# Optimization experiments

Hardware: AMD Instinct MI355X
Metric: run time of the kernel (lower is better)

The kernel has to match this reference:

```python
import jax, jax.numpy as jnp
import numpy as np

ACT_BITS = 8
W_BITS = 8
BN_EPS = 1e-5


def _round_ste(x):
    # straight-through round (HAWQ-style ste_round)
    return x + jax.lax.stop_gradient(jnp.round(x) - x)


def _quant_sym(x, bits):
    # symmetric per-tensor fake quantization; scale treated as constant (EMA min/max in original)
    n = float(2 ** (bits - 1) - 1)
    s = jax.lax.stop_gradient(jnp.maximum(jnp.max(jnp.abs(x)) / n, 1e-8))
    xq = jnp.clip(_round_ste(x / s), -n - 1.0, n) * s
    return xq, s


def _conv(x, w, stride, pad):
    return jax.lax.conv_general_dilated(
        x, w, (stride, stride), [(pad, pad), (pad, pad)],
        dimension_numbers=("NCHW", "OIHW", "NCHW"))


def _quant_bn(x, gamma, beta, mean, var):
    # fold BN into a per-channel scale+bias; quantize the folded scale like a weight
    ws = gamma * jax.lax.rsqrt(var + BN_EPS)          # [C]
    wq, ws_scale = _quant_sym(ws, W_BITS)
    b = beta - mean * wq                               # [C]
    return x * wq[None, :, None, None] + b[None, :, None, None], ws_scale


def setup_inputs() -> dict:
    key = jax.random.key(0)
    ks = jax.random.split(key, 16)
    d = {}
    d["x"] = jax.random.normal(ks[0], (32, 128, 56, 56), jnp.float32)
    d["w1"] = jax.random.normal(ks[1], (256, 128, 3, 3), jnp.float32) * 0.05
    d["w2"] = jax.random.normal(ks[2], (256, 256, 3, 3), jnp.float32) * 0.05
    d["w_id"] = jax.random.normal(ks[3], (256, 128, 1, 1), jnp.float32) * 0.05
    for i, pfx in enumerate(["bn1", "bn2", "id"]):
        k4 = jax.random.split(ks[4 + i], 4)
        d[pfx + "_gamma"] = jax.random.uniform(k4[0], (256,), jnp.float32) + 0.5
        d[pfx + "_beta"] = jax.random.normal(k4[1], (256,), jnp.float32) * 0.1
        d[pfx + "_mean"] = jax.random.normal(k4[2], (256,), jnp.float32) * 0.1
        d[pfx + "_var"] = jax.random.uniform(k4[3], (256,), jnp.float32) + 0.5
    return d


def reference(x, w1, w2, w_id,
              bn1_gamma, bn1_beta, bn1_mean, bn1_var,
              bn2_gamma, bn2_beta, bn2_mean, bn2_var,
              id_gamma, id_beta, id_mean, id_var):
    # quant_act on block input
    xq, act_s = _quant_sym(x, ACT_BITS)

    # identity branch: 1x1 stride-2 quantized conv -> quant_act -> folded quant bn
    w_id_q, _ = _quant_sym(w_id, W_BITS)
    identity = _conv(xq, w_id_q, 2, 0)
    identity, _ = _quant_sym(identity, ACT_BITS)
    identity, _ = _quant_bn(identity, id_gamma, id_beta, id_mean, id_var)

    # main branch conv1 (3x3 stride 2) -> act quant -> bn -> relu -> act quant
    w1_q, _ = _quant_sym(w1, W_BITS)
    h = _conv(xq, w1_q, 2, 1)
    h, _ = _quant_sym(h, ACT_BITS)
    h, _ = _quant_bn(h, bn1_gamma, bn1_beta, bn1_mean, bn1_var)
    h = jax.nn.relu(h)
    h, _ = _quant_sym(h, ACT_BITS)

    # conv2 (3x3 stride 1) -> act quant -> bn
    w2_q, _ = _quant_sym(w2, W_BITS)
    h = _conv(h, w2_q, 1, 1)
    h, _ = _quant_sym(h, ACT_BITS)
    h, _ = _quant_bn(h, bn2_gamma, bn2_beta, bn2_mean, bn2_var)

    # residual add -> int32 requant -> relu
    h = h + identity
    h, out_s = _quant_sym(h, ACT_BITS)
    h = jax.nn.relu(h)
    return h, out_s
```

## Files before the change

kernel.cpp:

```cpp
#include <hip/hip_runtime.h>
#include <limits.h>

#define THREADS 256
#define TAIL_BLOCKS 896

typedef int vi4 __attribute__((ext_vector_type(4)));

__device__ __forceinline__ float clamp8f(float q) { return fminf(fmaxf(q, -128.0f), 127.0f); }
__device__ __forceinline__ float sc_from_bits(unsigned b) {
  return fmaxf(__uint_as_float(b) / 127.0f, 1e-8f);
}
__device__ __forceinline__ signed char q8(float v, float s) {
  return (signed char)(int)clamp8f(rintf(v / s));
}


__device__ __forceinline__ void amax_body(const float4* __restrict__ p, int n4, int bid,
                                          int nblocks, int* __restrict__ slot) {
  const int tid = threadIdx.x;
  const int stride = nblocks * THREADS;
  float m = 0.0f;
  int i = bid * THREADS + tid;
  for (; i + 3 * stride < n4; i += 4 * stride) {
    float4 v0 = p[i];
    float4 v1 = p[i + stride];
    float4 v2 = p[i + 2 * stride];
    float4 v3 = p[i + 3 * stride];
    float m0 = fmaxf(fmaxf(fabsf(v0.x), fabsf(v0.y)), fmaxf(fabsf(v0.z), fabsf(v0.w)));
    float m1 = fmaxf(fmaxf(fabsf(v1.x), fabsf(v1.y)), fmaxf(fabsf(v1.z), fabsf(v1.w)));
    float m2 = fmaxf(fmaxf(fabsf(v2.x), fabsf(v2.y)), fmaxf(fabsf(v2.z), fabsf(v2.w)));
    float m3 = fmaxf(fmaxf(fabsf(v3.x), fabsf(v3.y)), fmaxf(fabsf(v3.z), fabsf(v3.w)));
    m = fmaxf(m, fmaxf(fmaxf(m0, m1), fmaxf(m2, m3)));
  }
  for (; i < n4; i += stride) {
    float4 v = p[i];
    m = fmaxf(m, fmaxf(fmaxf(fabsf(v.x), fabsf(v.y)), fmaxf(fabsf(v.z), fabsf(v.w))));
  }
#pragma unroll
  for (int k = 32; k >= 1; k >>= 1) m = fmaxf(m, __shfl_xor(m, k));
  __shared__ float wred[4];
  if ((tid & 63) == 0) wred[tid >> 6] = m;
  __syncthreads();
  if (tid == 0) {
    m = fmaxf(fmaxf(wred[0], wred[1]), fmaxf(wred[2], wred[3]));
    atomicMax(slot, __float_as_int(m));
  }
}

__global__ __launch_bounds__(THREADS) void k_pre(
    int* IS, const float* g1, const float* be1, const float* m1, const float* v1, float* wq1,
    float* b1, const float* g2, const float* be2, const float* m2, const float* v2, float* wq2,
    float* b2, const float* gi, const float* bei, const float* mi, const float* vvi, float* wqi,
    float* bi, const float4* w1, const float4* w2, const float4* wid, const float4* x) {
  int b = blockIdx.x;
  int c = threadIdx.x;
  if (b < 3) {
    const float *gamma, *beta, *mean, *var;
    float *wq, *bb;
    if (b == 0) { gamma = g1; beta = be1; mean = m1; var = v1; wq = wq1; bb = b1; }
    else if (b == 1) { gamma = g2; beta = be2; mean = m2; var = v2; wq = wq2; bb = b2; }
    else { gamma = gi; beta = bei; mean = mi; var = vvi; wq = wqi; bb = bi; }
    __shared__ float red[THREADS];
    float ws = gamma[c] * (1.0f / sqrtf(var[c] + 1e-5f));
    red[c] = fabsf(ws);
    __syncthreads();
    for (int s = THREADS / 2; s > 0; s >>= 1) {
      if (c < s) red[c] = fmaxf(red[c], red[c + s]);
      __syncthreads();
    }
    float sws = fmaxf(red[0] / 127.0f, 1e-8f);
    float q = clamp8f(rintf(ws / sws)) * sws;
    wq[c] = q;
    bb[c] = beta[c] - mean[c] * q;
    return;
  }
  b -= 3;
  if (b < 64) { amax_body(w1, 73728, b, 64, IS + 1); return; }
  b -= 64;
  if (b < 128) { amax_body(w2, 147456, b, 128, IS + 2); return; }
  b -= 128;
  if (b < 16) { amax_body(wid, 8192, b, 16, IS + 3); return; }
  b -= 16;
  amax_body(x, 3211264, b, 512, IS + 0);
}

__global__ __launch_bounds__(THREADS) void k_quant(const float* __restrict__ x,
                                                   int* __restrict__ X8,
                                                   const float* __restrict__ w1f,
                                                   vi4* __restrict__ W1m,
                                                   const float* __restrict__ w2f,
                                                   vi4* __restrict__ W2m,
                                                   const float* __restrict__ widf,
                                                   vi4* __restrict__ Widm,
                                                   const unsigned* __restrict__ ISu) {
  __shared__ signed char tile[56 * 132];
  int b = blockIdx.x;
  int t = threadIdx.x;
  if (b < 1792) {
    float s = sc_from_bits(ISu[0]);
    int h = b % 56, n = b / 56;
    const float* xp = x + ((n * 128) * 56 + h) * 56;
#pragma unroll
    for (int k = 0; k < 28; ++k) {
      int i = t + k * 256;
      int w = i % 56, c = i / 56;
      tile[w * 132 + c] = q8(xp[c * 3136 + w], s);
    }
    __syncthreads();
    int* op = X8 + (n * 56 + h) * 56 * 32;
#pragma unroll
    for (int k = 0; k < 7; ++k) {
      int i = t + k * 256;
      int w = i >> 5, c4 = (i & 31) * 4;
      const signed char* tp = tile + w * 132 + c4;
      op[i] = (int)(unsigned char)tp[0] | ((int)(unsigned char)tp[1] << 8) |
              ((int)(unsigned char)tp[2] << 16) | ((int)(unsigned char)tp[3] << 24);
    }
    return;
  }
  if (b < 1864) {
    int tt = (b - 1792) * THREADS + t;
    float s = sc_from_bits(ISu[1]);
    int lane = tt & 63;
    int cotile = (tt >> 6) & 15;
    int ks = tt >> 10;
    int tap = ks >> 1, kc = ks & 1;
    int kh = tap / 3, kw = tap % 3;
    int co = cotile * 16 + (lane & 15);
    int ci0 = kc * 64 + (lane >> 4) * 16;
    const float* src = w1f + (co * 128 + ci0) * 9 + kh * 3 + kw;
    int r[4];
#pragma unroll
    for (int q = 0; q < 4; ++q) {
      unsigned b0 = (unsigned char)q8(src[(q * 4 + 0) * 9], s);
      unsigned b1 = (unsigned char)q8(src[(q * 4 + 1) * 9], s);
      unsigned b2 = (unsigned char)q8(src[(q * 4 + 2) * 9], s);
      unsigned b3 = (unsigned char)q8(src[(q * 4 + 3) * 9], s);
      r[q] = (int)(b0 | (b1 << 8) | (b2 << 16) | (b3 << 24));
    }
    vi4 v = {r[0], r[1], r[2], r[3]};
    W1m[tt] = v;
    return;
  }
  if (b < 2008) {
    int tt = (b - 1864) * THREADS + t;
    float s = sc_from_bits(ISu[2]);
    int lane = tt & 63;
    int cotile = (tt >> 6) & 15;
    int ks = tt >> 10;
    int tap = ks >> 2, kc = ks & 3;
    int kh = tap / 3, kw = tap % 3;
    int co = cotile * 16 + (lane & 15);
    int ci0 = kc * 64 + (lane >> 4) * 16;
    const float* src = w2f + (co * 256 + ci0) * 9 + kh * 3 + kw;
    int r[4];
#pragma unroll
    for (int q = 0; q < 4; ++q) {
      unsigned b0 = (unsigned char)q8(src[(q * 4 + 0) * 9], s);
      unsigned b1 = (unsigned char)q8(src[(q * 4 + 1) * 9], s);
      unsigned b2 = (unsigned char)q8(src[(q * 4 + 2) * 9], s);
      unsigned b3 = (unsigned char)q8(src[(q * 4 + 3) * 9], s);
      r[q] = (int)(b0 | (b1 << 8) | (b2 << 16) | (b3 << 24));
    }
    vi4 v = {r[0], r[1], r[2], r[3]};
    W2m[tt] = v;
    return;
  }
  {
    int tt = (b - 2008) * THREADS + t;
    float s = sc_from_bits(ISu[3]);
    int lane = tt & 63;
    int cotile = (tt >> 6) & 15;
    int ks = tt >> 10;
    int co = cotile * 16 + (lane & 15);
    int ci0 = ks * 64 + (lane >> 4) * 16;
    const float* src = widf + co * 128 + ci0;
    int r[4];
#pragma unroll
    for (int q = 0; q < 4; ++q) {
      unsigned b0 = (unsigned char)q8(src[q * 4 + 0], s);
      unsigned b1 = (unsigned char)q8(src[q * 4 + 1], s);
      unsigned b2 = (unsigned char)q8(src[q * 4 + 2], s);
      unsigned b3 = (unsigned char)q8(src[q * 4 + 3], s);
      r[q] = (int)(b0 | (b1 << 8) | (b2 << 16) | (b3 << 24));
    }
    vi4 v = {r[0], r[1], r[2], r[3]};
    Widm[tt] = v;
  }
}

#define MFMA_I8(a, b, c) __builtin_amdgcn_mfma_i32_16x16x64_i8(a, b, c, 0, 0, 0)

__global__ __launch_bounds__(THREADS, 3) void k_conv1(const int* __restrict__ X8,
                                                      const vi4* __restrict__ W1m,
                                                      const vi4* __restrict__ Widm,
                                                      int* __restrict__ H1, int* __restrict__ IDI,
                                                      int* __restrict__ maxS,
                                                      int* __restrict__ minS,
                                                      int* __restrict__ maxabs_id) {
  __shared__ __align__(16) int lds[5 * 58 * 36];
  __shared__ int sMax[2][128], sMin[2][128], redA[4];
  const int tid = threadIdx.x;
  const int bx = blockIdx.x;
  const int n = bx / 28, rr = bx % 28;
  const int hp = rr >> 1, nh = rr & 1;
  const int ho0 = hp * 2;
  vi4 zero = {0, 0, 0, 0};

  for (int r = 0; r < 5; ++r) {
    int h = 2 * ho0 - 1 + r;
    int* dst = lds + r * 58 * 36;
    if (h >= 0 && h < 56) {
      const vi4* src = (const vi4*)(X8 + (n * 56 + h) * 56 * 32);
      for (int i4 = tid; i4 < 448; i4 += THREADS) {
        int col = i4 >> 3, c = (i4 & 7) * 4;
        *(vi4*)(dst + (col + 1) * 36 + c) = src[i4];
      }
      if (tid < 32) dst[tid] = 0;
      else if (tid >= 128 && tid < 160) dst[57 * 36 + (tid - 128)] = 0;
    } else {
      for (int i4 = tid; i4 < 522; i4 += THREADS) ((vi4*)dst)[i4] = zero;
    }
  }
  __syncthreads();

  const int lane = tid & 63, wv = tid >> 6;
  const int mw = wv & 1, nw = wv >> 1;
  const int lm = lane & 15, quad = lane >> 4;
  const int woc0 = lm, woc1 = (16 + lm) > 27 ? 27 : (16 + lm);
  const int choff = quad * 4;
  const int ho = ho0 + mw;
  const int obase = ((n * 28 + ho) * 28) * 256;
  const int ctbase = nh * 8 + nw * 4;

  vi4 acc[2][4];
  vi4 bA[4], bB[4];
  vi4 a0A, a1A, a0B, a1B;

#pragma unroll
  for (int mt = 0; mt < 2; ++mt)
#pragma unroll
    for (int ct = 0; ct < 4; ++ct) acc[mt][ct] = zero;
  const vi4* wibase = Widm + ctbase * 64 + lane;
  {
    const int ro = (2 * mw + 1) * 58;
#pragma unroll
    for (int kc = 0; kc < 2; ++kc) {
      vi4 a0 = *(const vi4*)(lds + (ro + 2 * woc0 + 1) * 36 + kc * 16 + choff);
      vi4 a1 = *(const vi4*)(lds + (ro + 2 * woc1 + 1) * 36 + kc * 16 + choff);
#pragma unroll
      for (int ct = 0; ct < 4; ++ct) {
        vi4 b = wibase[kc * 1024 + ct * 64];
        acc[0][ct] = MFMA_I8(a0, b, acc[0][ct]);
        acc[1][ct] = MFMA_I8(a1, b, acc[1][ct]);
      }
    }
  }
  int am = 0;
#pragma unroll
  for (int ct = 0; ct < 4; ++ct) {
    const int co = (ctbase + ct) * 16 + lm;
#pragma unroll
    for (int mt = 0; mt < 2; ++mt)
#pragma unroll
      for (int r = 0; r < 4; ++r) {
        int wo = mt * 16 + quad * 4 + r;
        if (wo < 28) {
          int v = acc[mt][ct][r];
          IDI[obase + wo * 256 + co] = v;
          am = max(am, v < 0 ? -v : v);
        }
      }
  }
#pragma unroll
  for (int k = 32; k >= 1; k >>= 1) am = max(am, __shfl_xor(am, k));
  if (lane == 0) redA[wv] = am;

#pragma unroll
  for (int mt = 0; mt < 2; ++mt)
#pragma unroll
    for (int ct = 0; ct < 4; ++ct) acc[mt][ct] = zero;
  const vi4* wbase = W1m + ctbase * 64 + lane;
#pragma unroll
  for (int ct = 0; ct < 4; ++ct) bA[ct] = wbase[ct * 64];
  {
    const int ro = (2 * mw) * 58;
    a0A = *(const vi4*)(lds + (ro + 2 * woc0) * 36 + choff);
    a1A = *(const vi4*)(lds + (ro + 2 * woc1) * 36 + choff);
  }
#pragma unroll 1
  for (int ks = 0; ks < 18; ks += 2) {
    {
      const int ksn = ks + 1;
      const int khn = (ksn >= 6) + (ksn >= 12);
      const int t2 = ksn - khn * 6;
      const int kwn = t2 >> 1, kcn = t2 & 1;
#pragma unroll
      for (int ct = 0; ct < 4; ++ct) bB[ct] = wbase[ksn * 1024 + ct * 64];
      const int ro = (2 * mw + khn) * 58;
      a0B = *(const vi4*)(lds + (ro + 2 * woc0 + kwn) * 36 + kcn * 16 + choff);
      a1B = *(const vi4*)(lds + (ro + 2 * woc1 + kwn) * 36 + kcn * 16 + choff);
    }
#pragma unroll
    for (int ct = 0; ct < 4; ++ct) {
      acc[0][ct] = MFMA_I8(a0A, bA[ct], acc[0][ct]);
      acc[1][ct] = MFMA_I8(a1A, bA[ct], acc[1][ct]);
    }
    if (ks + 2 < 18) {
      const int ksn = ks + 2;
      const int khn = (ksn >= 6) + (ksn >= 12);
      const int t2 = ksn - khn * 6;
      const int kwn = t2 >> 1, kcn = t2 & 1;
#pragma unroll
      for (int ct = 0; ct < 4; ++ct) bA[ct] = wbase[ksn * 1024 + ct * 64];
      const int ro = (2 * mw + khn) * 58;
      a0A = *(const vi4*)(lds + (ro + 2 * woc0 + kwn) * 36 + kcn * 16 + choff);
      a1A = *(const vi4*)(lds + (ro + 2 * woc1 + kwn) * 36 + kcn * 16 + choff);
    }
#pragma unroll
    for (int ct = 0; ct < 4; ++ct) {
      acc[0][ct] = MFMA_I8(a0B, bB[ct], acc[0][ct]);
      acc[1][ct] = MFMA_I8(a1B, bB[ct], acc[1][ct]);
    }
  }

#pragma unroll
  for (int ct = 0; ct < 4; ++ct) {
    const int co = (ctbase + ct) * 16 + lm;
    int vmax = INT_MIN, vmin = INT_MAX;
#pragma unroll
    for (int mt = 0; mt < 2; ++mt)
#pragma unroll
      for (int r = 0; r < 4; ++r) {
        int wo = mt * 16 + quad * 4 + r;
        if (wo < 28) {
          int v = acc[mt][ct][r];
          H1[obase + wo * 256 + co] = v;
          vmax = max(vmax, v);
          vmin = min(vmin, v);
        }
      }
    vmax = max(vmax, __shfl_xor(vmax, 16));
    vmax = max(vmax, __shfl_xor(vmax, 32));
    vmin = min(vmin, __shfl_xor(vmin, 16));
    vmin = min(vmin, __shfl_xor(vmin, 32));
    if (lane < 16) {
      sMax[mw][nw * 64 + ct * 16 + lane] = vmax;
      sMin[mw][nw * 64 + ct * 16 + lane] = vmin;
    }
  }
  __syncthreads();
  if (tid < 128) {
    int row = n * 14 + hp;
    maxS[row * 256 + nh * 128 + tid] = max(sMax[0][tid], sMax[1][tid]);
    minS[row * 256 + nh * 128 + tid] = min(sMin[0][tid], sMin[1][tid]);
  }
  if (tid == 0) {
    int a = max(max(redA[0], redA[1]), max(redA[2], redA[3]));
    atomicMax(maxabs_id, a);
  }
}

__global__ __launch_bounds__(1024) void k_rs1(int* __restrict__ IS, float* __restrict__ SC,
                                              const int* __restrict__ maxS,
                                              const int* __restrict__ minS,
                                              const float* __restrict__ wq1,
                                              const float* __restrict__ b1) {
  __shared__ int pMax[4][256], pMin[4][256];
  __shared__ int ri[256];
  __shared__ float rf[256];
  int t = threadIdx.x;
  if (t < 320) IS[128 + t] = 0;
  int c = t & 255, part = t >> 8;
  int vmax = INT_MIN, vmin = INT_MAX;
#pragma unroll 4
  for (int r = part; r < 448; r += 4) {
    vmax = max(vmax, maxS[r * 256 + c]);
    vmin = min(vmin, minS[r * 256 + c]);
  }
  pMax[part][c] = vmax;
  pMin[part][c] = vmin;
  __syncthreads();
  if (t < 256) {
    vmax = max(max(pMax[0][c], pMax[1][c]), max(pMax[2][c], pMax[3][c]));
    vmin = min(min(pMin[0][c], pMin[1][c]), min(pMin[2][c], pMin[3][c]));
    int a1 = vmax < 0 ? -vmax : vmax;
    int a0 = vmin < 0 ? -vmin : vmin;
    ri[c] = max(a1, a0);
  }
  __syncthreads();
  for (int s = 128; s > 0; s >>= 1) {
    if (t < s) ri[t] = max(ri[t], ri[t + s]);
    __syncthreads();
  }
  int mh1 = ri[0];
  const unsigned* ISu = (const unsigned*)IS;
  float sx = sc_from_bits(ISu[0]);
  float sw1 = sc_from_bits(ISu[1]);
  float sxw = sx * sw1;
  float s_h1 = fmaxf(sxw * (float)mh1 / 127.0f, 1e-8f);
  if (t < 256) {
    float wq = wq1[c], bbc = b1[c];
    float q1 = clamp8f(rintf((float)vmax * sxw / s_h1));
    float q0 = clamp8f(rintf((float)vmin * sxw / s_h1));
    float hv1 = q1 * s_h1, hv0 = q0 * s_h1;
    float y1 = fmaxf(hv1 * wq + bbc, 0.0f);
    float y0 = fmaxf(hv0 * wq + bbc, 0.0f);
    rf[c] = fmaxf(y1, y0);
  }
  __syncthreads();
  for (int s = 128; s > 0; s >>= 1) {
    if (t < s) rf[t] = fmaxf(rf[t], rf[t + s]);
    __syncthreads();
  }
  if (t == 0) {
    IS[4] = mh1;
    SC[7] = rf[0];
    SC[8] = s_h1;
    SC[9] = fmaxf(rf[0] / 127.0f, 1e-8f);
    float swid = sc_from_bits(ISu[3]);
    SC[10] = fmaxf(sx * swid * (float)IS[5] / 127.0f, 1e-8f);
  }
}

__device__ __forceinline__ signed char qact(int v, float sxw, float s_h1, float s_y2, float wq,
                                            float bb) {
  float hf = (float)v * sxw;
  float q = clamp8f(rintf(hf / s_h1));
  float hv = q * s_h1;
  float y = fmaxf(hv * wq + bb, 0.0f);
  float a = fminf(fmaxf(rintf(y / s_y2), -128.0f), 127.0f);
  return (signed char)(int)a;
}

__global__ __launch_bounds__(THREADS) void k_qh1(const int4* __restrict__ H1,
                                                 char4* __restrict__ A2,
                                                 const float* __restrict__ SC,
                                                 const float* __restrict__ wq1,
                                                 const float* __restrict__ b1) {
  int t = blockIdx.x * THREADS + threadIdx.x;
  const unsigned* ISu = (const unsigned*)SC;
  float sx = sc_from_bits(ISu[0]);
  float sw1 = sc_from_bits(ISu[1]);
  float sxw = sx * sw1;
  float s_h1 = SC[8];
  float s_y2 = SC[9];
  int4 v = H1[t];
  int c0 = (t * 4) & 255;
  char4 r;
  r.x = qact(v.x, sxw, s_h1, s_y2, wq1[c0], b1[c0]);
  r.y = qact(v.y, sxw, s_h1, s_y2, wq1[c0 + 1], b1[c0 + 1]);
  r.z = qact(v.z, sxw, s_h1, s_y2, wq1[c0 + 2], b1[c0 + 2]);
  r.w = qact(v.w, sxw, s_h1, s_y2, wq1[c0 + 3], b1[c0 + 3]);
  A2[t] = r;
}

struct SumParams {
  float sxw2, s_h2, sxwid, s_idq;
};
__device__ __forceinline__ float sum_val(int v2, int vi, const SumParams& P, float wq2c, float b2c,
                                         float wqidc, float bidc) {
  float q2 = clamp8f(rintf((float)v2 * P.sxw2 / P.s_h2));
  float z = (q2 * P.s_h2) * wq2c + b2c;
  float qi = clamp8f(rintf((float)vi * P.sxwid / P.s_idq));
  float zi = (qi * P.s_idq) * wqidc + bidc;
  return z + zi;
}
__device__ __forceinline__ SumParams make_params2(const float* SC, const unsigned* ISu, int mh2) {
  SumParams P;
  float sx = sc_from_bits(ISu[0]);
  float sw2 = sc_from_bits(ISu[2]);
  float swid = sc_from_bits(ISu[3]);
  float s_y2 = SC[9];
  P.s_idq = SC[10];
  P.sxw2 = s_y2 * sw2;
  P.s_h2 = fmaxf(P.sxw2 * (float)mh2 / 127.0f, 1e-8f);
  P.sxwid = sx * swid;
  return P;
}

__global__ __launch_bounds__(THREADS, 4) void k_tail(const int* __restrict__ A2,
                                                     const vi4* __restrict__ W2m,
                                                     const int* __restrict__ IDI,
                                                     const float* SC, int* IS,
                                                     const float* __restrict__ wq2,
                                                     const float* __restrict__ b2,
                                                     const float* __restrict__ wqid,
                                                     const float* __restrict__ bidp,
                                                     float* __restrict__ out) {
  __shared__ __align__(16) int lds[4 * 30 * 68];
  __shared__ int redA[4];
  __shared__ float redF[4];
  __shared__ int sMh2;
  __shared__ float sOutS;
  const int tid = threadIdx.x;
  const int bx = blockIdx.x;
  const int n = bx / 28, rr = bx % 28;
  const int hp = rr >> 1, nh = rr & 1;
  const int ho0 = hp * 2;
  vi4 zero = {0, 0, 0, 0};

  for (int r = 0; r < 4; ++r) {
    int h = ho0 - 1 + r;
    int* dst = lds + r * 30 * 68;
    if (h >= 0 && h < 28) {
      const vi4* src = (const vi4*)(A2 + (n * 28 + h) * 28 * 64);
      for (int i4 = tid; i4 < 448; i4 += THREADS) {
        int col = i4 >> 4, c = (i4 & 15) * 4;
        *(vi4*)(dst + (col + 1) * 68 + c) = src[i4];
      }
      if (tid < 64) dst[tid] = 0;
      else if (tid >= 128 && tid < 192) dst[29 * 68 + (tid - 128)] = 0;
    } else {
      for (int i4 = tid; i4 < 510; i4 += THREADS) ((vi4*)dst)[i4] = zero;
    }
  }
  __syncthreads();

  const int lane = tid & 63, wv = tid >> 6;
  const int mw = wv & 1, nw = wv >> 1;
  const int lm = lane & 15, quad = lane >> 4;
  const int woc0 = lm, woc1 = (16 + lm) > 27 ? 27 : (16 + lm);
  const int choff = quad * 4;
  const int ctbase = nh * 8 + nw * 4;

  vi4 acc[2][4];
  vi4 bA[4], bB[4];
  vi4 a0A, a1A, a0B, a1B;
#pragma unroll
  for (int mt = 0; mt < 2; ++mt)
#pragma unroll
    for (int ct = 0; ct < 4; ++ct) acc[mt][ct] = zero;

  const vi4* wbase = W2m + ctbase * 64 + lane;
#pragma unroll
  for (int ct = 0; ct < 4; ++ct) bA[ct] = wbase[ct * 64];
  {
    const int ro = mw * 30;
    a0A = *(const vi4*)(lds + (ro + woc0) * 68 + choff);
    a1A = *(const vi4*)(lds + (ro + woc1) * 68 + choff);
  }
#pragma unroll 1
  for (int ks = 0; ks < 36; ks += 2) {
    {
      const int ksn = ks + 1;
      const int khn = (ksn >= 12) + (ksn >= 24);
      const int t2 = ksn - khn * 12;
      const int kwn = t2 >> 2, kcn = t2 & 3;
#pragma unroll
      for (int ct = 0; ct < 4; ++ct) bB[ct] = wbase[ksn * 1024 + ct * 64];
      const int ro = (mw + khn) * 30;
      a0B = *(const vi4*)(lds + (ro + woc0 + kwn) * 68 + kcn * 16 + choff);
      a1B = *(const vi4*)(lds + (ro + woc1 + kwn) * 68 + kcn * 16 + choff);
    }
#pragma unroll
    for (int ct = 0; ct < 4; ++ct) {
      acc[0][ct] = MFMA_I8(a0A, bA[ct], acc[0][ct]);
      acc[1][ct] = MFMA_I8(a1A, bA[ct], acc[1][ct]);
    }
    if (ks + 2 < 36) {
      const int ksn = ks + 2;
      const int khn = (ksn >= 12) + (ksn >= 24);
      const int t2 = ksn - khn * 12;
      const int kwn = t2 >> 2, kcn = t2 & 3;
#pragma unroll
      for (int ct = 0; ct < 4; ++ct) bA[ct] = wbase[ksn * 1024 + ct * 64];
      const int ro = (mw + khn) * 30;
      a0A = *(const vi4*)(lds + (ro + woc0 + kwn) * 68 + kcn * 16 + choff);
      a1A = *(const vi4*)(lds + (ro + woc1 + kwn) * 68 + kcn * 16 + choff);
    }
#pragma unroll
    for (int ct = 0; ct < 4; ++ct) {
      acc[0][ct] = MFMA_I8(a0B, bB[ct], acc[0][ct]);
      acc[1][ct] = MFMA_I8(a1B, bB[ct], acc[1][ct]);
    }
  }

  int am = 0;
#pragma unroll
  for (int ct = 0; ct < 4; ++ct)
#pragma unroll
    for (int mt = 0; mt < 2; ++mt)
#pragma unroll
      for (int r = 0; r < 4; ++r) {
        int wo = mt * 16 + quad * 4 + r;
        if (wo < 28) {
          int v = acc[mt][ct][r];
          am = max(am, v < 0 ? -v : v);
        }
      }
#pragma unroll
  for (int k = 32; k >= 1; k >>= 1) am = max(am, __shfl_xor(am, k));
  if (lane == 0) redA[wv] = am;
  __syncthreads();
  if (tid == 0) {
    int a = max(max(redA[0], redA[1]), max(redA[2], redA[3]));
    atomicMax(IS + 6, a);
  }

  int* sumsi = lds;
  float* sums = (float*)lds;
  const int ib = ((n * 28 + ho0) * 28) * 256 + nh * 128;
#pragma unroll
  for (int k = 0; k < 28; ++k) {
    int idx = tid + k * 256;
    int cl = idx & 127, sp = idx >> 7;
    sumsi[cl * 57 + sp] = IDI[ib + sp * 256 + cl];
  }
  __syncthreads();

  if (tid == 0) {
    asm volatile("s_waitcnt vmcnt(0)" ::: "memory");
    int old = __hip_atomic_fetch_add(IS + 128 + (bx & 7) * 16, 1, __ATOMIC_RELAXED,
                                     __HIP_MEMORY_SCOPE_AGENT);
    if (old == 111) {
      int r = __hip_atomic_fetch_add(IS + 256, 1, __ATOMIC_RELAXED, __HIP_MEMORY_SCOPE_AGENT);
      if (r == 7)
        __hip_atomic_fetch_add(IS + 272, 1, __ATOMIC_RELAXED, __HIP_MEMORY_SCOPE_AGENT);
    }
    while (__hip_atomic_load(IS + 272, __ATOMIC_RELAXED, __HIP_MEMORY_SCOPE_SYSTEM) == 0)
      __builtin_amdgcn_s_sleep(2);
    sMh2 = __hip_atomic_load(IS + 6, __ATOMIC_RELAXED, __HIP_MEMORY_SCOPE_SYSTEM);
  }
  __syncthreads();
  const SumParams P = make_params2(SC, (const unsigned*)IS, sMh2);

  float fm = 0.0f;
#pragma unroll
  for (int ct = 0; ct < 4; ++ct) {
    const int co = (ctbase + ct) * 16 + lm;
    const int cl = co - nh * 128;
    float w2c = wq2[co], b2c = b2[co], wic = wqid[co], bic = bidp[co];
#pragma unroll
    for (int mt = 0; mt < 2; ++mt)
#pragma unroll
      for (int r = 0; r < 4; ++r) {
        int wo = mt * 16 + quad * 4 + r;
        if (wo < 28) {
          int slot = cl * 57 + mw * 28 + wo;
          float sv = sum_val(acc[mt][ct][r], sumsi[slot], P, w2c, b2c, wic, bic);
          sums[slot] = sv;
          fm = fmaxf(fm, fabsf(sv));
        }
      }
  }
#pragma unroll
  for (int k = 32; k >= 1; k >>= 1) fm = fmaxf(fm, __shfl_xor(fm, k));
  if (lane == 0) redF[wv] = fm;
  __syncthreads();

  if (tid == 0) {
    float a = fmaxf(fmaxf(redF[0], redF[1]), fmaxf(redF[2], redF[3]));
    atomicMax(IS + 11, __float_as_int(a));
    asm volatile("s_waitcnt vmcnt(0)" ::: "memory");
    int old = __hip_atomic_fetch_add(IS + 288 + (bx & 7) * 16, 1, __ATOMIC_RELAXED,
                                     __HIP_MEMORY_SCOPE_AGENT);
    if (old == 111) {
      int r = __hip_atomic_fetch_add(IS + 416, 1, __ATOMIC_RELAXED, __HIP_MEMORY_SCOPE_AGENT);
      if (r == 7)
        __hip_atomic_fetch_add(IS + 432, 1, __ATOMIC_RELAXED, __HIP_MEMORY_SCOPE_AGENT);
    }
    while (__hip_atomic_load(IS + 432, __ATOMIC_RELAXED, __HIP_MEMORY_SCOPE_SYSTEM) == 0)
      __builtin_amdgcn_s_sleep(2);
    int mb = __hip_atomic_load(IS + 11, __ATOMIC_RELAXED, __HIP_MEMORY_SCOPE_SYSTEM);
    sOutS = fmaxf(__int_as_float(mb) / 127.0f, 1e-8f);
  }
  __syncthreads();
  const float out_s = sOutS;

  float* ob = out + n * 200704 + (nh * 128) * 784 + ho0 * 28;
#pragma unroll
  for (int k = 0; k < 28; ++k) {
    int idx = tid + k * 256;
    int cl = idx / 56, rem = idx % 56;
    float sv = sums[cl * 57 + rem];
    float q = clamp8f(rintf(sv / out_s));
    ob[cl * 784 + rem] = q > 0.0f ? q * out_s : 0.0f;
  }
  if (bx == 0 && tid == 0) out[6422528] = out_s;
}

extern "C" void kernel_launch(void* const* d_in, const int* in_sizes, int n_in, void* d_out,
                              int out_size, void* d_ws, size_t ws_size, hipStream_t stream) {
  (void)in_sizes; (void)n_in; (void)out_size; (void)ws_size;
  const float* x = (const float*)d_in[0];
  const float* w1 = (const float*)d_in[1];
  const float* w2 = (const float*)d_in[2];
  const float* wid = (const float*)d_in[3];
  const float* bn1g = (const float*)d_in[4];
  const float* bn1b = (const float*)d_in[5];
  const float* bn1m = (const float*)d_in[6];
  const float* bn1v = (const float*)d_in[7];
  const float* bn2g = (const float*)d_in[8];
  const float* bn2b = (const float*)d_in[9];
  const float* bn2m = (const float*)d_in[10];
  const float* bn2v = (const float*)d_in[11];
  const float* idg = (const float*)d_in[12];
  const float* idb = (const float*)d_in[13];
  const float* idm = (const float*)d_in[14];
  const float* idv = (const float*)d_in[15];

  char* ws = (char*)d_ws;
  float* SC = (float*)ws;
  int* IS = (int*)ws;
  unsigned* ISu = (unsigned*)ws;
  float* wq1 = (float*)(ws + 3072);
  float* b1 = (float*)(ws + 4096);
  float* wq2 = (float*)(ws + 5120);
  float* b2 = (float*)(ws + 6144);
  float* wqid = (float*)(ws + 7168);
  float* bid = (float*)(ws + 8192);
  char* X8 = ws + 16384;
  char* A2 = X8;
  char* W1m = X8 + 12845056;
  char* W2m = W1m + 294912;
  char* Widm = W2m + 589824;
  int* H1 = (int*)(Widm + 32768);
  int* IDI = (int*)((char*)H1 + 25690112);
  float* out = (float*)d_out;
  int* maxS = (int*)d_out;
  int* minS = maxS + 448 * 256;

  k_pre<<<723, THREADS, 0, stream>>>(IS, bn1g, bn1b, bn1m, bn1v, wq1, b1, bn2g, bn2b, bn2m, bn2v,
                                     wq2, b2, idg, idb, idm, idv, wqid, bid, (const float4*)w1,
                                     (const float4*)w2, (const float4*)wid, (const float4*)x);
  k_quant<<<2016, THREADS, 0, stream>>>(x, (int*)X8, w1, (vi4*)W1m, w2, (vi4*)W2m, wid,
                                        (vi4*)Widm, ISu);
  k_conv1<<<896, THREADS, 0, stream>>>((const int*)X8, (const vi4*)W1m, (const vi4*)Widm, H1, IDI,
                                       maxS, minS, IS + 5);
  k_rs1<<<1, 1024, 0, stream>>>(IS, SC, maxS, minS, wq1, b1);
  k_qh1<<<6272, THREADS, 0, stream>>>((const int4*)H1, (char4*)A2, SC, wq1, b1);
  k_tail<<<TAIL_BLOCKS, THREADS, 0, stream>>>((const int*)A2, (const vi4*)W2m, (const int*)IDI, SC,
                                              IS, wq2, b2, wqid, bid, out);
}
```

Measured before the change: 249.5 us.

## Fuse conv1, scale reduction and activation requant into one persistent kernel

Merges k_conv1, k_rs1 and k_qh1 into a single 896-block kernel that keeps the int32 conv1 outputs in LDS, uses software grid barriers to compute the per-channel min/max and the activation scales, then writes the int8 A2 tensor directly. This removes the 25 MB H1 int32 round-trip through global memory and two kernel launches, including a single-block reduction kernel. The LDS input tile also switches from padded rows to an XOR-swizzled layout, and occupancy is raised to 4 blocks per SM. The cost is three grid-wide spin barriers, which depend on all 896 blocks being co-resident and can deadlock if they are not.

Measured after the change: 246.9 us. No clear change (-1.0%).

```diff
diff --git a/kernel.cpp b/kernel.cpp
--- a/kernel.cpp
+++ b/kernel.cpp
@@ -2,7 +2,7 @@
 #include <limits.h>
 
 #define THREADS 256
-#define TAIL_BLOCKS 896
+#define GRID_BLOCKS 896
 
 typedef int vi4 __attribute__((ext_vector_type(4)));
 
@@ -14,6 +14,19 @@
   return (signed char)(int)clamp8f(rintf(v / s));
 }
 
+
+__device__ __forceinline__ void gbar(int* IS, int base, int bx) {
+  asm volatile("s_waitcnt vmcnt(0)" ::: "memory");
+  int old = __hip_atomic_fetch_add(IS + base + (bx & 7) * 16, 1, __ATOMIC_RELAXED,
+                                   __HIP_MEMORY_SCOPE_AGENT);
+  if (old == 111) {
+    int r = __hip_atomic_fetch_add(IS + base + 128, 1, __ATOMIC_RELAXED, __HIP_MEMORY_SCOPE_AGENT);
+    if (r == 7)
+      __hip_atomic_fetch_add(IS + base + 144, 1, __ATOMIC_RELAXED, __HIP_MEMORY_SCOPE_AGENT);
+  }
+  while (__hip_atomic_load(IS + base + 144, __ATOMIC_RELAXED, __HIP_MEMORY_SCOPE_SYSTEM) == 0)
+    __builtin_amdgcn_s_sleep(2);
+}
 
 __device__ __forceinline__ void amax_body(const float4* __restrict__ p, int n4, int bid,
                                           int nblocks, int* __restrict__ slot) {
@@ -55,6 +68,12 @@
   int b = blockIdx.x;
   int c = threadIdx.x;
   if (b < 3) {
+    if (b == 0) {
+      IS[128 + c] = 0;
+      IS[384 + c] = 0;
+      IS[640 + c] = 0;
+      if (c < 32) IS[896 + c] = 0;
+    }
     const float *gamma, *beta, *mean, *var;
     float *wq, *bb;
     if (b == 0) { gamma = g1; beta = be1; mean = m1; var = v1; wq = wq1; bb = b1; }
@@ -191,15 +210,26 @@
 
 #define MFMA_I8(a, b, c) __builtin_amdgcn_mfma_i32_16x16x64_i8(a, b, c, 0, 0, 0)
 
-__global__ __launch_bounds__(THREADS, 3) void k_conv1(const int* __restrict__ X8,
-                                                      const vi4* __restrict__ W1m,
-                                                      const vi4* __restrict__ Widm,
-                                                      int* __restrict__ H1, int* __restrict__ IDI,
-                                                      int* __restrict__ maxS,
-                                                      int* __restrict__ minS,
-                                                      int* __restrict__ maxabs_id) {
-  __shared__ __align__(16) int lds[5 * 58 * 36];
-  __shared__ int sMax[2][128], sMin[2][128], redA[4];
+__device__ __forceinline__ signed char qact(int v, float sxw, float s_h1, float s_y2, float wq,
+                                            float bb) {
+  float hf = (float)v * sxw;
+  float q = clamp8f(rintf(hf / s_h1));
+  float hv = q * s_h1;
+  float y = fmaxf(hv * wq + bb, 0.0f);
+  float a = fminf(fmaxf(rintf(y / s_y2), -128.0f), 127.0f);
+  return (signed char)(int)a;
+}
+
+__global__ __launch_bounds__(THREADS, 4) void k_cv1(const int* X8, const vi4* __restrict__ W1m,
+                                                    const vi4* __restrict__ Widm,
+                                                    int* __restrict__ IDI, int* A2i, int* IS,
+                                                    const float* __restrict__ wq1,
+                                                    const float* __restrict__ b1, float* SC,
+                                                    int* maxS2, int* minS2) {
+  __shared__ __align__(16) int lds[9280];
+  __shared__ int redA[4];
+  __shared__ int sVmax, sVmin;
+  __shared__ float sSxw, sSh1, sSy2;
   const int tid = threadIdx.x;
   const int bx = blockIdx.x;
   const int n = bx / 28, rr = bx % 28;
@@ -209,17 +239,18 @@
 
   for (int r = 0; r < 5; ++r) {
     int h = 2 * ho0 - 1 + r;
-    int* dst = lds + r * 58 * 36;
+    int* dst = lds + r * 58 * 32;
     if (h >= 0 && h < 56) {
       const vi4* src = (const vi4*)(X8 + (n * 56 + h) * 56 * 32);
       for (int i4 = tid; i4 < 448; i4 += THREADS) {
-        int col = i4 >> 3, c = (i4 & 7) * 4;
-        *(vi4*)(dst + (col + 1) * 36 + c) = src[i4];
+        int col = i4 >> 3, e0 = (i4 & 7) * 4;
+        int cell = r * 58 + col + 1;
+        *(vi4*)(lds + cell * 32 + (e0 ^ ((cell & 7) << 2))) = src[i4];
       }
       if (tid < 32) dst[tid] = 0;
-      else if (tid >= 128 && tid < 160) dst[57 * 36 + (tid - 128)] = 0;
+      else if (tid >= 128 && tid < 160) dst[57 * 32 + (tid - 128)] = 0;
     } else {
-      for (int i4 = tid; i4 < 522; i4 += THREADS) ((vi4*)dst)[i4] = zero;
+      for (int i4 = tid; i4 < 464; i4 += THREADS) ((vi4*)dst)[i4] = zero;
     }
   }
   __syncthreads();
@@ -233,6 +264,10 @@
   const int obase = ((n * 28 + ho) * 28) * 256;
   const int ctbase = nh * 8 + nw * 4;
 
+#define LDA(row, colp, sub)                                                              \
+  (*(const vi4*)(lds + ((row) * 58 + (colp)) * 32 +                                      \
+                 ((sub) ^ ((((row) * 58 + (colp)) & 7) << 2))))
+
   vi4 acc[2][4];
   vi4 bA[4], bB[4];
   vi4 a0A, a1A, a0B, a1B;
@@ -243,11 +278,11 @@
     for (int ct = 0; ct < 4; ++ct) acc[mt][ct] = zero;
   const vi4* wibase = Widm + ctbase * 64 + lane;
   {
-    const int ro = (2 * mw + 1) * 58;
+    const int row = 2 * mw + 1;
 #pragma unroll
     for (int kc = 0; kc < 2; ++kc) {
-      vi4 a0 = *(const vi4*)(lds + (ro + 2 * woc0 + 1) * 36 + kc * 16 + choff);
-      vi4 a1 = *(const vi4*)(lds + (ro + 2 * woc1 + 1) * 36 + kc * 16 + choff);
+      vi4 a0 = LDA(row, 2 * woc0 + 1, kc * 16 + choff);
+      vi4 a1 = LDA(row, 2 * woc1 + 1, kc * 16 + choff);
 #pragma unroll
       for (int ct = 0; ct < 4; ++ct) {
         vi4 b = wibase[kc * 1024 + ct * 64];
@@ -284,9 +319,8 @@
 #pragma unroll
   for (int ct = 0; ct < 4; ++ct) bA[ct] = wbase[ct * 64];
   {
-    const int ro = (2 * mw) * 58;
-    a0A = *(const vi4*)(lds + (ro + 2 * woc0) * 36 + choff);
-    a1A = *(const vi4*)(lds + (ro + 2 * woc1) * 36 + choff);
+    a0A = LDA(2 * mw, 2 * woc0, choff);
+    a1A = LDA(2 * mw, 2 * woc1, choff);
   }
 #pragma unroll 1
   for (int ks = 0; ks < 18; ks += 2) {
@@ -297,9 +331,9 @@
       const int kwn = t2 >> 1, kcn = t2 & 1;
 #pragma unroll
       for (int ct = 0; ct < 4; ++ct) bB[ct] = wbase[ksn * 1024 + ct * 64];
-      const int ro = (2 * mw + khn) * 58;
-      a0B = *(const vi4*)(lds + (ro + 2 * woc0 + kwn) * 36 + kcn * 16 + choff);
-      a1B = *(const vi4*)(lds + (ro + 2 * woc1 + kwn) * 36 + kcn * 16 + choff);
+      const int row = 2 * mw + khn;
+      a0B = LDA(row, 2 * woc0 + kwn, kcn * 16 + choff);
+      a1B = LDA(row, 2 * woc1 + kwn, kcn * 16 + choff);
     }
 #pragma unroll
     for (int ct = 0; ct < 4; ++ct) {
@@ -313,9 +347,9 @@
       const int kwn = t2 >> 1, kcn = t2 & 1;
 #pragma unroll
       for (int ct = 0; ct < 4; ++ct) bA[ct] = wbase[ksn * 1024 + ct * 64];
-      const int ro = (2 * mw + khn) * 58;
-      a0A = *(const vi4*)(lds + (ro + 2 * woc0 + kwn) * 36 + kcn * 16 + choff);
-      a1A = *(const vi4*)(lds + (ro + 2 * woc1 + kwn) * 36 + kcn * 16 + choff);
+      const int row = 2 * mw + khn;
+      a0A = LDA(row, 2 * woc0 + kwn, kcn * 16 + choff);
+      a1A = LDA(row, 2 * woc1 + kwn, kcn * 16 + choff);
     }
 #pragma unroll
     for (int ct = 0; ct < 4; ++ct) {
@@ -326,7 +360,6 @@
 
 #pragma unroll
   for (int ct = 0; ct < 4; ++ct) {
-    const int co = (ctbase + ct) * 16 + lm;
     int vmax = INT_MIN, vmin = INT_MAX;
 #pragma unroll
     for (int mt = 0; mt < 2; ++mt)
@@ -335,7 +368,6 @@
         int wo = mt * 16 + quad * 4 + r;
         if (wo < 28) {
           int v = acc[mt][ct][r];
-          H1[obase + wo * 256 + co] = v;
           vmax = max(vmax, v);
           vmin = min(vmin, v);
         }
@@ -345,114 +377,132 @@
     vmin = min(vmin, __shfl_xor(vmin, 16));
     vmin = min(vmin, __shfl_xor(vmin, 32));
     if (lane < 16) {
-      sMax[mw][nw * 64 + ct * 16 + lane] = vmax;
-      sMin[mw][nw * 64 + ct * 16 + lane] = vmin;
-    }
-  }
-  __syncthreads();
-  if (tid < 128) {
-    int row = n * 14 + hp;
-    maxS[row * 256 + nh * 128 + tid] = max(sMax[0][tid], sMax[1][tid]);
-    minS[row * 256 + nh * 128 + tid] = min(sMin[0][tid], sMin[1][tid]);
-  }
+      int cl = (nw * 4 + ct) * 16 + lane;
+      __hip_atomic_store(maxS2 + bx * 256 + mw * 128 + cl, vmax, __ATOMIC_RELAXED,
+                         __HIP_MEMORY_SCOPE_AGENT);
+      __hip_atomic_store(minS2 + bx * 256 + mw * 128 + cl, vmin, __ATOMIC_RELAXED,
+                         __HIP_MEMORY_SCOPE_AGENT);
+    }
+  }
+
+  __syncthreads();
   if (tid == 0) {
     int a = max(max(redA[0], redA[1]), max(redA[2], redA[3]));
-    atomicMax(maxabs_id, a);
-  }
-}
-
-__global__ __launch_bounds__(1024) void k_rs1(int* __restrict__ IS, float* __restrict__ SC,
-                                              const int* __restrict__ maxS,
-                                              const int* __restrict__ minS,
-                                              const float* __restrict__ wq1,
-                                              const float* __restrict__ b1) {
-  __shared__ int pMax[4][256], pMin[4][256];
-  __shared__ int ri[256];
-  __shared__ float rf[256];
-  int t = threadIdx.x;
-  if (t < 320) IS[128 + t] = 0;
-  int c = t & 255, part = t >> 8;
-  int vmax = INT_MIN, vmin = INT_MAX;
-#pragma unroll 4
-  for (int r = part; r < 448; r += 4) {
-    vmax = max(vmax, maxS[r * 256 + c]);
-    vmin = min(vmin, minS[r * 256 + c]);
-  }
-  pMax[part][c] = vmax;
-  pMin[part][c] = vmin;
-  __syncthreads();
-  if (t < 256) {
-    vmax = max(max(pMax[0][c], pMax[1][c]), max(pMax[2][c], pMax[3][c]));
-    vmin = min(min(pMin[0][c], pMin[1][c]), min(pMin[2][c], pMin[3][c]));
-    int a1 = vmax < 0 ? -vmax : vmax;
-    int a0 = vmin < 0 ? -vmin : vmin;
-    ri[c] = max(a1, a0);
-  }
-  __syncthreads();
-  for (int s = 128; s > 0; s >>= 1) {
-    if (t < s) ri[t] = max(ri[t], ri[t + s]);
+    atomicMax(IS + 5, a);
+  }
+#pragma unroll
+  for (int ct = 0; ct < 4; ++ct) {
+    const int cl = (nw * 4 + ct) * 16 + lm;
+#pragma unroll
+    for (int mt = 0; mt < 2; ++mt)
+#pragma unroll
+      for (int r = 0; r < 4; ++r) {
+        int wo = mt * 16 + quad * 4 + r;
+        if (wo < 28) lds[(mw * 28 + wo) * 130 + cl] = acc[mt][ct][r];
+      }
+  }
+  __syncthreads();
+  if (tid == 0) gbar(IS, 128, bx);
+  __syncthreads();
+
+  if (bx < 256) {
+    const int c = bx, nhc = c >> 7, cl = c & 127;
+    int vmax = INT_MIN, vmin = INT_MAX;
+    for (int j = tid; j < 896; j += THREADS) {
+      int bxx = nhc + ((j >> 1) << 1);
+      int mwj = j & 1;
+      int a = __hip_atomic_load(maxS2 + bxx * 256 + mwj * 128 + cl, __ATOMIC_RELAXED,
+                                __HIP_MEMORY_SCOPE_AGENT);
+      int i_ = __hip_atomic_load(minS2 + bxx * 256 + mwj * 128 + cl, __ATOMIC_RELAXED,
+                                 __HIP_MEMORY_SCOPE_AGENT);
+      vmax = max(vmax, a);
+      vmin = min(vmin, i_);
+    }
+    int* rMax = lds + 7280;
+    int* rMin = lds + 7536;
+    rMax[tid] = vmax;
+    rMin[tid] = vmin;
     __syncthreads();
-  }
-  int mh1 = ri[0];
-  const unsigned* ISu = (const unsigned*)IS;
-  float sx = sc_from_bits(ISu[0]);
-  float sw1 = sc_from_bits(ISu[1]);
-  float sxw = sx * sw1;
-  float s_h1 = fmaxf(sxw * (float)mh1 / 127.0f, 1e-8f);
-  if (t < 256) {
-    float wq = wq1[c], bbc = b1[c];
-    float q1 = clamp8f(rintf((float)vmax * sxw / s_h1));
-    float q0 = clamp8f(rintf((float)vmin * sxw / s_h1));
-    float hv1 = q1 * s_h1, hv0 = q0 * s_h1;
-    float y1 = fmaxf(hv1 * wq + bbc, 0.0f);
-    float y0 = fmaxf(hv0 * wq + bbc, 0.0f);
-    rf[c] = fmaxf(y1, y0);
-  }
-  __syncthreads();
-  for (int s = 128; s > 0; s >>= 1) {
-    if (t < s) rf[t] = fmaxf(rf[t], rf[t + s]);
-    __syncthreads();
-  }
-  if (t == 0) {
-    IS[4] = mh1;
-    SC[7] = rf[0];
-    SC[8] = s_h1;
-    SC[9] = fmaxf(rf[0] / 127.0f, 1e-8f);
-    float swid = sc_from_bits(ISu[3]);
-    SC[10] = fmaxf(sx * swid * (float)IS[5] / 127.0f, 1e-8f);
-  }
-}
-
-__device__ __forceinline__ signed char qact(int v, float sxw, float s_h1, float s_y2, float wq,
-                                            float bb) {
-  float hf = (float)v * sxw;
-  float q = clamp8f(rintf(hf / s_h1));
-  float hv = q * s_h1;
-  float y = fmaxf(hv * wq + bb, 0.0f);
-  float a = fminf(fmaxf(rintf(y / s_y2), -128.0f), 127.0f);
-  return (signed char)(int)a;
-}
-
-__global__ __launch_bounds__(THREADS) void k_qh1(const int4* __restrict__ H1,
-                                                 char4* __restrict__ A2,
-                                                 const float* __restrict__ SC,
-                                                 const float* __restrict__ wq1,
-                                                 const float* __restrict__ b1) {
-  int t = blockIdx.x * THREADS + threadIdx.x;
-  const unsigned* ISu = (const unsigned*)SC;
-  float sx = sc_from_bits(ISu[0]);
-  float sw1 = sc_from_bits(ISu[1]);
-  float sxw = sx * sw1;
-  float s_h1 = SC[8];
-  float s_y2 = SC[9];
-  int4 v = H1[t];
-  int c0 = (t * 4) & 255;
-  char4 r;
-  r.x = qact(v.x, sxw, s_h1, s_y2, wq1[c0], b1[c0]);
-  r.y = qact(v.y, sxw, s_h1, s_y2, wq1[c0 + 1], b1[c0 + 1]);
-  r.z = qact(v.z, sxw, s_h1, s_y2, wq1[c0 + 2], b1[c0 + 2]);
-  r.w = qact(v.w, sxw, s_h1, s_y2, wq1[c0 + 3], b1[c0 + 3]);
-  A2[t] = r;
+    for (int s = 128; s > 0; s >>= 1) {
+      if (tid < s) {
+        rMax[tid] = max(rMax[tid], rMax[tid + s]);
+        rMin[tid] = min(rMin[tid], rMin[tid + s]);
+      }
+      __syncthreads();
+    }
+    if (tid == 0) {
+      sVmax = rMax[0];
+      sVmin = rMin[0];
+      int a1 = sVmax < 0 ? -sVmax : sVmax;
+      int a0 = sVmin < 0 ? -sVmin : sVmin;
+      atomicMax(IS + 4, max(a1, a0));
+    }
+  }
+  __syncthreads();
+  if (tid == 0) gbar(IS, 288, bx);
+  __syncthreads();
+
+  if (bx < 256 && tid == 0) {
+    float sx = sc_from_bits((unsigned)__hip_atomic_load(IS + 0, __ATOMIC_RELAXED,
+                                                        __HIP_MEMORY_SCOPE_AGENT));
+    float sw1 = sc_from_bits((unsigned)__hip_atomic_load(IS + 1, __ATOMIC_RELAXED,
+                                                         __HIP_MEMORY_SCOPE_AGENT));
+    int mh1 = __hip_atomic_load(IS + 4, __ATOMIC_RELAXED, __HIP_MEMORY_SCOPE_AGENT);
+    float sxw = sx * sw1;
+    float s_h1 = fmaxf(sxw * (float)mh1 / 127.0f, 1e-8f);
+    float wq = wq1[bx], bbc = b1[bx];
+    float q1 = clamp8f(rintf((float)sVmax * sxw / s_h1));
+    float q0 = clamp8f(rintf((float)sVmin * sxw / s_h1));
+    float y1 = fmaxf(q1 * s_h1 * wq + bbc, 0.0f);
+    float y0 = fmaxf(q0 * s_h1 * wq + bbc, 0.0f);
+    atomicMax(IS + 7, __float_as_int(fmaxf(y1, y0)));
+  }
+  __syncthreads();
+  if (tid == 0) gbar(IS, 448, bx);
+  __syncthreads();
+
+  if (tid == 0) {
+    float sx = sc_from_bits((unsigned)__hip_atomic_load(IS + 0, __ATOMIC_RELAXED,
+                                                        __HIP_MEMORY_SCOPE_AGENT));
+    float sw1 = sc_from_bits((unsigned)__hip_atomic_load(IS + 1, __ATOMIC_RELAXED,
+                                                         __HIP_MEMORY_SCOPE_AGENT));
+    int mh1 = __hip_atomic_load(IS + 4, __ATOMIC_RELAXED, __HIP_MEMORY_SCOPE_AGENT);
+    int mrf = __hip_atomic_load(IS + 7, __ATOMIC_RELAXED, __HIP_MEMORY_SCOPE_AGENT);
+    float sxw = sx * sw1;
+    float s_h1 = fmaxf(sxw * (float)mh1 / 127.0f, 1e-8f);
+    float s_y2 = fmaxf(__int_as_float(mrf) / 127.0f, 1e-8f);
+    sSxw = sxw;
+    sSh1 = s_h1;
+    sSy2 = s_y2;
+    if (bx == 0) {
+      int mid = __hip_atomic_load(IS + 5, __ATOMIC_RELAXED, __HIP_MEMORY_SCOPE_AGENT);
+      float swid = sc_from_bits((unsigned)__hip_atomic_load(IS + 3, __ATOMIC_RELAXED,
+                                                            __HIP_MEMORY_SCOPE_AGENT));
+      SC[9] = s_y2;
+      SC[10] = fmaxf(sx * swid * (float)mid / 127.0f, 1e-8f);
+    }
+  }
+  __syncthreads();
+
+  {
+    const float sxw = sSxw, s_h1 = sSh1, s_y2 = sSy2;
+#pragma unroll
+    for (int k = 0; k < 7; ++k) {
+      int i = tid + k * 256;
+      int sp = i >> 5, c4i = i & 31;
+      int mwp = sp >= 28 ? 1 : 0;
+      int wo = sp - mwp * 28;
+      int c0 = nh * 128 + c4i * 4;
+      const int* pk = lds + sp * 130 + c4i * 4;
+      unsigned r0 = (unsigned char)qact(pk[0], sxw, s_h1, s_y2, wq1[c0], b1[c0]);
+      unsigned r1 = (unsigned char)qact(pk[1], sxw, s_h1, s_y2, wq1[c0 + 1], b1[c0 + 1]);
+      unsigned r2 = (unsigned char)qact(pk[2], sxw, s_h1, s_y2, wq1[c0 + 2], b1[c0 + 2]);
+      unsigned r3 = (unsigned char)qact(pk[3], sxw, s_h1, s_y2, wq1[c0 + 3], b1[c0 + 3]);
+      A2i[((n * 28 + ho0 + mwp) * 28 + wo) * 64 + nh * 32 + c4i] =
+          (int)(r0 | (r1 << 8) | (r2 << 16) | (r3 << 24));
+    }
+  }
+#undef LDA
 }
 
 struct SumParams {
@@ -608,18 +658,8 @@
     sumsi[cl * 57 + sp] = IDI[ib + sp * 256 + cl];
   }
   __syncthreads();
-
   if (tid == 0) {
-    asm volatile("s_waitcnt vmcnt(0)" ::: "memory");
-    int old = __hip_atomic_fetch_add(IS + 128 + (bx & 7) * 16, 1, __ATOMIC_RELAXED,
-                                     __HIP_MEMORY_SCOPE_AGENT);
-    if (old == 111) {
-      int r = __hip_atomic_fetch_add(IS + 256, 1, __ATOMIC_RELAXED, __HIP_MEMORY_SCOPE_AGENT);
-      if (r == 7)
-        __hip_atomic_fetch_add(IS + 272, 1, __ATOMIC_RELAXED, __HIP_MEMORY_SCOPE_AGENT);
-    }
-    while (__hip_atomic_load(IS + 272, __ATOMIC_RELAXED, __HIP_MEMORY_SCOPE_SYSTEM) == 0)
-      __builtin_amdgcn_s_sleep(2);
+    gbar(IS, 608, bx);
     sMh2 = __hip_atomic_load(IS + 6, __ATOMIC_RELAXED, __HIP_MEMORY_SCOPE_SYSTEM);
   }
   __syncthreads();
@@ -648,20 +688,10 @@
   for (int k = 32; k >= 1; k >>= 1) fm = fmaxf(fm, __shfl_xor(fm, k));
   if (lane == 0) redF[wv] = fm;
   __syncthreads();
-
   if (tid == 0) {
     float a = fmaxf(fmaxf(redF[0], redF[1]), fmaxf(redF[2], redF[3]));
     atomicMax(IS + 11, __float_as_int(a));
-    asm volatile("s_waitcnt vmcnt(0)" ::: "memory");
-    int old = __hip_atomic_fetch_add(IS + 288 + (bx & 7) * 16, 1, __ATOMIC_RELAXED,
-                                     __HIP_MEMORY_SCOPE_AGENT);
-    if (old == 111) {
-      int r = __hip_atomic_fetch_add(IS + 416, 1, __ATOMIC_RELAXED, __HIP_MEMORY_SCOPE_AGENT);
-      if (r == 7)
-        __hip_atomic_fetch_add(IS + 432, 1, __ATOMIC_RELAXED, __HIP_MEMORY_SCOPE_AGENT);
-    }
-    while (__hip_atomic_load(IS + 432, __ATOMIC_RELAXED, __HIP_MEMORY_SCOPE_SYSTEM) == 0)
-      __builtin_amdgcn_s_sleep(2);
+    gbar(IS, 768, bx);
     int mb = __hip_atomic_load(IS + 11, __ATOMIC_RELAXED, __HIP_MEMORY_SCOPE_SYSTEM);
     sOutS = fmaxf(__int_as_float(mb) / 127.0f, 1e-8f);
   }
@@ -704,32 +734,29 @@
   float* SC = (float*)ws;
   int* IS = (int*)ws;
   unsigned* ISu = (unsigned*)ws;
-  float* wq1 = (float*)(ws + 3072);
-  float* b1 = (float*)(ws + 4096);
-  float* wq2 = (float*)(ws + 5120);
-  float* b2 = (float*)(ws + 6144);
-  float* wqid = (float*)(ws + 7168);
-  float* bid = (float*)(ws + 8192);
+  float* wq1 = (float*)(ws + 4096);
+  float* b1 = (float*)(ws + 5120);
+  float* wq2 = (float*)(ws + 6144);
+  float* b2 = (float*)(ws + 7168);
+  float* wqid = (float*)(ws + 8192);
+  float* bid = (float*)(ws + 9216);
   char* X8 = ws + 16384;
   char* A2 = X8;
   char* W1m = X8 + 12845056;
   char* W2m = W1m + 294912;
   char* Widm = W2m + 589824;
-  int* H1 = (int*)(Widm + 32768);
-  int* IDI = (int*)((char*)H1 + 25690112);
+  int* IDI = (int*)(Widm + 32768);
   float* out = (float*)d_out;
-  int* maxS = (int*)d_out;
-  int* minS = maxS + 448 * 256;
+  int* maxS2 = (int*)d_out;
+  int* minS2 = maxS2 + 896 * 256;
 
   k_pre<<<723, THREADS, 0, stream>>>(IS, bn1g, bn1b, bn1m, bn1v, wq1, b1, bn2g, bn2b, bn2m, bn2v,
                                      wq2, b2, idg, idb, idm, idv, wqid, bid, (const float4*)w1,
                                      (const float4*)w2, (const float4*)wid, (const float4*)x);
   k_quant<<<2016, THREADS, 0, stream>>>(x, (int*)X8, w1, (vi4*)W1m, w2, (vi4*)W2m, wid,
                                         (vi4*)Widm, ISu);
-  k_conv1<<<896, THREADS, 0, stream>>>((const int*)X8, (const vi4*)W1m, (const vi4*)Widm, H1, IDI,
-                                       maxS, minS, IS + 5);
-  k_rs1<<<1, 1024, 0, stream>>>(IS, SC, maxS, minS, wq1, b1);
-  k_qh1<<<6272, THREADS, 0, stream>>>((const int4*)H1, (char4*)A2, SC, wq1, b1);
-  k_tail<<<TAIL_BLOCKS, THREADS, 0, stream>>>((const int*)A2, (const vi4*)W2m, (const int*)IDI, SC,
+  k_cv1<<<GRID_BLOCKS, THREADS, 0, stream>>>((const int*)X8, (const vi4*)W1m, (const vi4*)Widm,
+                                             IDI, (int*)A2, IS, wq1, b1, SC, maxS2, minS2);
+  k_tail<<<GRID_BLOCKS, THREADS, 0, stream>>>((const int*)A2, (const vi4*)W2m, (const int*)IDI, SC,
                                               IS, wq2, b2, wqid, bid, out);
 }
```
